# Optimization experiments

Measured on AMD Instinct MI355X. Metric: run time of the kernel, lower is better.

Reference implementation:

```python
import jax, jax.numpy as jnp
from jax import lax
import numpy as np

DN = ('NCHW', 'OIHW', 'NCHW')

def conv(x, w, b, stride, pad):
    y = lax.conv_general_dilated(x, w, (stride, stride), [(pad, pad), (pad, pad)], dimension_numbers=DN)
    return y + b[None, :, None, None]

def conv_t(x, w, b, stride, pad):
    # PyTorch ConvTranspose2d weight layout is (in, out, kh, kw); flip spatially, swap to OIHW,
    # and realize transpose-conv as lhs-dilated conv with padding k-1-p.
    k = w.shape[2]
    wt = jnp.flip(w, (2, 3)).transpose(1, 0, 2, 3)
    q = k - 1 - pad
    y = lax.conv_general_dilated(x, wt, (1, 1), [(q, q), (q, q)], lhs_dilation=(stride, stride), dimension_numbers=DN)
    return y + b[None, :, None, None]

def setup_inputs() -> dict:
    key = jax.random.key(0)
    ks = jax.random.split(key, 16)
    K, C = 512, 64
    def he(k, shape, fan_in):
        return jax.random.normal(k, shape, jnp.float32) * np.float32(np.sqrt(2.0 / fan_in))
    return {
        'x': jax.random.normal(ks[0], (64, 1, 256, 256), jnp.float32),
        'e1_w': he(ks[1], (32, 1, 4, 4), 1 * 16), 'e1_b': jnp.zeros((32,), jnp.float32),
        'e2_w': he(ks[2], (64, 32, 4, 4), 32 * 16), 'e2_b': jnp.zeros((64,), jnp.float32),
        'e3_w': he(ks[3], (64, 64, 3, 3), 64 * 9), 'e3_b': jnp.zeros((64,), jnp.float32),
        'emb': jax.random.uniform(ks[4], (K, C), jnp.float32, -1.0 / K, 1.0 / K),
        'd1_w': he(ks[5], (64, 32, 3, 3), 64 * 9), 'd1_b': jnp.zeros((32,), jnp.float32),
        'd2_w': he(ks[6], (32, 64, 4, 4), 32 * 16), 'd2_b': jnp.zeros((64,), jnp.float32),
        'd3_w': he(ks[7], (64, 1, 4, 4), 64 * 16), 'd3_b': jnp.zeros((1,), jnp.float32),
    }

def reference(x, e1_w, e1_b, e2_w, e2_b, e3_w, e3_b, emb, d1_w, d1_b, d2_w, d2_b, d3_w, d3_b):
    # encoder
    h = jax.nn.relu(conv(x, e1_w, e1_b, 2, 1))
    h = jax.nn.relu(conv(h, e2_w, e2_b, 2, 1))
    ze = jax.nn.relu(conv(h, e3_w, e3_b, 1, 1))  # (N, C, H, W)
    N, C, H, W = ze.shape
    # VQ: nearest codebook entry per spatial location via ||z||^2 - 2 z.e + ||e||^2
    zf = ze.transpose(0, 2, 3, 1).reshape(-1, C)  # (N*H*W, C)
    dist = (zf * zf).sum(-1, keepdims=True) - 2.0 * (zf @ emb.T) + (emb * emb).sum(-1)[None, :]
    idx = jnp.argmin(dist, axis=1)  # (N*H*W,)
    zq = emb[idx].reshape(N, H, W, C).transpose(0, 3, 1, 2)  # (N, C, H, W)
    # straight-through estimator
    dec_in = ze + lax.stop_gradient(zq - ze)
    # decoder
    h = jax.nn.relu(conv_t(dec_in, d1_w, d1_b, 1, 1))
    h = jax.nn.relu(conv_t(h, d2_w, d2_b, 2, 1))
    x_hat = conv_t(h, d3_w, d3_b, 2, 1)
    return (x_hat, ze, zq)
```

## Files before the change

### kernel.cpp

```cpp
#include <hip/hip_runtime.h>

typedef short short8 __attribute__((ext_vector_type(8)));
typedef float f32x4 __attribute__((ext_vector_type(4)));

union U8 { short8 s8; unsigned int u[4]; };

__device__ __forceinline__ unsigned short f2bf(float f) {
    unsigned int u = __float_as_uint(f);
    u = (u + 0x7fffu + ((u >> 16) & 1u)) >> 16;
    return (unsigned short)u;
}
__device__ __forceinline__ float bf2f(unsigned short s) {
    return __uint_as_float(((unsigned int)s) << 16);
}


__global__ __launch_bounds__(256) void k_e1i(
    const float* __restrict__ x, const float* __restrict__ e1w, const float* __restrict__ e1b,
    unsigned short* __restrict__ h1p2, unsigned int* __restrict__ ws_dw,
    const float* __restrict__ e2w, const float* __restrict__ e3w,
    const float* __restrict__ d1w, const float* __restrict__ d2w,
    const float* __restrict__ d3w, const float* __restrict__ emb,
    unsigned short* __restrict__ ape2, unsigned short* __restrict__ ape3,
    unsigned short* __restrict__ apd1, unsigned short* __restrict__ apd2,
    unsigned short* __restrict__ apd3, unsigned short* __restrict__ embbf,
    float* __restrict__ hninit)
{
    int bid = blockIdx.x;
    if (bid < 4096) {
        int idx = bid * 256 + threadIdx.x;
        int ow = idx & 127, oh = (idx >> 7) & 127, n = idx >> 14;
        const float* xn = x + (size_t)n * 65536;
        float patch[16];
#pragma unroll
        for (int kh = 0; kh < 4; kh++) {
            int ih = 2 * oh + kh - 1;
#pragma unroll
            for (int kw = 0; kw < 4; kw++) {
                int iw = 2 * ow + kw - 1;
                bool ok = ((unsigned)ih < 256u) & ((unsigned)iw < 256u);
                patch[kh * 4 + kw] = ok ? xn[ih * 256 + iw] : 0.f;
            }
        }
        unsigned int outw[16];
#pragma unroll
        for (int oc = 0; oc < 32; oc++) {
            float acc = e1b[oc];
#pragma unroll
            for (int t = 0; t < 16; t++) acc += patch[t] * e1w[oc * 16 + t];
            unsigned short bf = f2bf(fmaxf(acc, 0.f));
            if (oc & 1) outw[oc >> 1] |= ((unsigned int)bf) << 16;
            else        outw[oc >> 1] = bf;
        }
        int par = ow & 1;
        int cidx = (ow + par) >> 1;
        size_t base = ((size_t)((idx >> 14) * 130 + oh + 1) * 2 + par) * 2112 + cidx * 32;
        uint4* dst = (uint4*)(h1p2 + base);
#pragma unroll
        for (int i = 0; i < 4; i++) dst[i] = *(uint4*)&outw[i * 4];
        return;
    }
    if (bid < 11376) {
        int t = (bid - 4096) * 256 + threadIdx.x;
        if (t < 270336) {
            int img = t / 4224, q = t % 4224;
            int rowsel = q / 2112, rem = q % 2112;
            ws_dw[img * 274560 + rowsel * 129 * 2112 + rem] = 0u;
        } else if (t < 532480) {
            int g = t - 270336;
            int img = g / 4096, q = g % 4096;
            int row = 1 + (q >> 5), c2 = q & 31;
            int sel = c2 >> 4, ch = c2 & 15;
            int par = sel ? 0 : 1, idx2 = sel ? 64 : 0;
            ws_dw[img * 274560 + row * 2112 + par * 1056 + idx2 * 16 + ch] = 0u;
        } else if (t < 1863680) {
            unsigned int base, Cd, r;
            if (t < 1064960)      { base = 17571840u; Cd = 32; r = t - 532480;  }
            else if (t < 1597440) { base = 34881536u; Cd = 32; r = t - 1064960; }
            else                  { base = 43802624u; Cd = 16; r = t - 1597440; }
            unsigned int per_img = 260u * Cd;
            unsigned int img = r / per_img, q = r % per_img;
            unsigned int p = q / Cd, c = q % Cd;
            unsigned int row, col;
            if (p < 66u)        { row = 0;  col = p; }
            else if (p < 132u)  { row = 65; col = p - 66u; }
            else { unsigned int s = p - 132u; row = 1 + (s >> 1); col = (s & 1) ? 65u : 0u; }
            ws_dw[base + ((img * 66u + row) * 66u + col) * Cd + c] = 0u;
        }
        return;
    }
    int f = (bid - 11376) * 256 + threadIdx.x;
    if (f < 4096) {
        int ks = f >> 8, mt = (f >> 6) & 3, lane = f & 63;
        int quad = lane >> 4, l16 = lane & 15;
        int oc = mt * 16 + l16, kh = ks >> 2, kw = ks & 3;
        short8 sv;
#pragma unroll
        for (int j = 0; j < 8; j++) {
            int ic = quad * 8 + j;
            sv[j] = (short)f2bf(e2w[((oc * 32 + ic) * 4 + kh) * 4 + kw]);
        }
        ((short8*)ape2)[f] = sv;
    } else if (f < 8704) {
        int g = f - 4096;
        int ks = g >> 8, mt = (g >> 6) & 3, lane = g & 63;
        int quad = lane >> 4, l16 = lane & 15;
        int oc = mt * 16 + l16, tap = ks >> 1, kh = tap / 3, kw = tap % 3;
        int icb = (ks & 1) * 32 + quad * 8;
        short8 sv;
#pragma unroll
        for (int j = 0; j < 8; j++)
            sv[j] = (short)f2bf(e3w[((oc * 64 + icb + j) * 3 + kh) * 3 + kw]);
        ((short8*)ape3)[g] = sv;
    } else if (f < 11008) {
        int g = f - 8704;
        int ks = g >> 7, mt = (g >> 6) & 1, lane = g & 63;
        int quad = lane >> 4, l16 = lane & 15;
        int oc = mt * 16 + l16, tap = ks >> 1, kh = tap / 3, kw = tap % 3;
        int icb = (ks & 1) * 32 + quad * 8;
        short8 sv;
#pragma unroll
        for (int j = 0; j < 8; j++)
            sv[j] = (short)f2bf(d1w[(((icb + j) * 32 + oc) * 3 + (2 - kh)) * 3 + (2 - kw)]);
        ((short8*)apd1)[g] = sv;
    } else if (f < 15104) {
        int g = f - 11008;
        int par = g >> 10, ks = (g >> 8) & 3, mt = (g >> 6) & 3, lane = g & 63;
        int quad = lane >> 4, l16 = lane & 15;
        int ph = par >> 1, pw = par & 1, a = ks >> 1, bb = ks & 1;
        int kh = 3 - ph - 2 * a, kw = 3 - pw - 2 * bb;
        int oc = mt * 16 + l16;
        short8 sv;
#pragma unroll
        for (int j = 0; j < 8; j++) {
            int ic = quad * 8 + j;
            sv[j] = (short)f2bf(d2w[((ic * 64 + oc) * 4 + kh) * 4 + kw]);
        }
        ((short8*)apd2)[g] = sv;
    } else if (f < 15232) {
        int g = f - 15104;
        int ks = g >> 6, lane = g & 63;
        int quad = lane >> 4, tap = lane & 15;
        short8 sv;
#pragma unroll
        for (int j = 0; j < 8; j++) {
            int ic = ks * 32 + quad * 8 + j;
            sv[j] = (short)f2bf(d3w[ic * 16 + tap]);
        }
        ((short8*)apd3)[g] = sv;
    } else if (f < 19328) {
        int g = f - 15232;
        int code = g >> 3, chb = (g & 7) * 8;
        short8 sv;
#pragma unroll
        for (int j = 0; j < 8; j++) sv[j] = (short)f2bf(emb[code * 64 + chb + j]);
        ((short8*)embbf)[g] = sv;
    } else if (f < 19840) {
        int code = f - 19328;
        float s = 0.f;
        for (int c = 0; c < 64; c++) { float v = emb[code * 64 + c]; s += v * v; }
        hninit[code] = 2.0f - 0.5f * s;
    }
}

template<int CIN, int COUT, int KSTEPS, int NCH, int WPIN, int MODE>
__global__ __launch_bounds__(256, 4) void k_conv(const unsigned short* __restrict__ inp,
                                                 const unsigned short* __restrict__ aprep,
                                                 const float* __restrict__ bias,
                                                 unsigned short* __restrict__ out0) {
    constexpr int MT = COUT / 16;
    constexpr int KCH = KSTEPS / NCH;
    __shared__ short8 sA[KCH * MT * 64];
    int tid = threadIdx.x;
    int wave = tid >> 6, lane = tid & 63, quad = lane >> 4, l16 = lane & 15;
    int bid = blockIdx.x;
    int n = bid >> 4, rg = bid & 15;
    int oh = rg * 4 + wave;

    int base0;
    if (MODE == 0) base0 = (n * 130 + 2 * oh) * 4224 + quad * 8;
    else           base0 = n * (WPIN * WPIN * CIN) + ((oh + 1) * WPIN + 1) * CIN + quad * 8;

    f32x4 acc[4][MT];
#pragma unroll
    for (int t = 0; t < 4; t++)
#pragma unroll
        for (int mt = 0; mt < MT; mt++)
            acc[t][mt] = *(const f32x4*)(bias + mt * 16 + quad * 4);

#pragma unroll
    for (int ch = 0; ch < NCH; ch++) {
        for (int i = tid; i < KCH * MT * 64; i += 256)
            sA[i] = ((const short8*)aprep)[ch * (KCH * MT * 64) + i];
        __syncthreads();
#pragma unroll
        for (int k = 0; k < KCH; k++) {
            int ks = ch * KCH + k;
            int off, pxs;
            if (MODE == 0) {
                int kh = ks >> 2, kw = ks & 3;
                int par = (kw & 1) ^ 1;
                off = kh * 4224 + par * 2112 + (kw >> 1) * 32;
                pxs = 32;
            } else {
                int tap = ks >> 1, kh = tap / 3, kw = tap % 3;
                off = ((kh - 1) * WPIN + (kw - 1)) * CIN + (ks & 1) * 32;
                pxs = CIN;
            }
            short8 bfr[4];
#pragma unroll
            for (int t = 0; t < 4; t++)
                bfr[t] = *(const short8*)(inp + base0 + (t * 16 + l16) * pxs + off);
#pragma unroll
            for (int mt = 0; mt < MT; mt++) {
                short8 a = sA[(k * MT + mt) * 64 + lane];
#pragma unroll
                for (int t = 0; t < 4; t++)
                    acc[t][mt] = __builtin_amdgcn_mfma_f32_16x16x32_bf16(a, bfr[t], acc[t][mt], 0, 0, 0);
            }
        }
        if (ch + 1 < NCH) __syncthreads();
    }

#pragma unroll
    for (int t = 0; t < 4; t++) {
        int ow = t * 16 + l16;
#pragma unroll
        for (int mt = 0; mt < MT; mt++) {
            float v0 = fmaxf(acc[t][mt][0], 0.f), v1 = fmaxf(acc[t][mt][1], 0.f);
            float v2 = fmaxf(acc[t][mt][2], 0.f), v3 = fmaxf(acc[t][mt][3], 0.f);
            unsigned int lo = (unsigned int)f2bf(v0) | ((unsigned int)f2bf(v1) << 16);
            unsigned int hi = (unsigned int)f2bf(v2) | ((unsigned int)f2bf(v3) << 16);
            uint2 uu; uu.x = lo; uu.y = hi;
            int oc = mt * 16 + quad * 4;
            if (MODE == 0) {
                size_t addr = (size_t)n * 278784 + ((oh + 1) * 66 + ow + 1) * 64 + oc;
                *(uint2*)(out0 + addr) = uu;
            } else {
                size_t addr = (size_t)n * 139392 + ((oh + 1) * 66 + ow + 1) * 32 + oc;
                *(uint2*)(out0 + addr) = uu;
            }
        }
    }
}

__global__ __launch_bounds__(256, 5) void k_e3vq(const unsigned short* __restrict__ h2p,
                                                 const unsigned short* __restrict__ ape3,
                                                 const float* __restrict__ bias,
                                                 const unsigned short* __restrict__ embbf,
                                                 const float* __restrict__ hninit,
                                                 float* __restrict__ ze_out,
                                                 float* __restrict__ zq_out,
                                                 unsigned short* __restrict__ zqp) {
    int tid = threadIdx.x;
    int wave = tid >> 6, lane = tid & 63, quad = lane >> 4, l16 = lane & 15;
    int bid = blockIdx.x;
    int n = bid >> 5, rg = (bid >> 1) & 15, half = bid & 1;
    int oh = rg * 4 + wave;
    int c0 = half * 32;
    int base0 = n * 278784 + ((oh + 1) * 66 + 1 + c0) * 64 + quad * 8;
    const short8* A = (const short8*)ape3;

    f32x4 acc[2][4];
#pragma unroll
    for (int t = 0; t < 2; t++)
#pragma unroll
        for (int mt = 0; mt < 4; mt++)
            acc[t][mt] = *(const f32x4*)(bias + mt * 16 + quad * 4);

#pragma unroll
    for (int ks = 0; ks < 18; ks++) {
        int tap = ks >> 1, kh = tap / 3, kw = tap % 3;
        int off = ((kh - 1) * 66 + (kw - 1)) * 64 + (ks & 1) * 32;
        short8 bfr[2];
#pragma unroll
        for (int t = 0; t < 2; t++)
            bfr[t] = *(const short8*)(h2p + base0 + (t * 16 + l16) * 64 + off);
#pragma unroll
        for (int mt = 0; mt < 4; mt++) {
            short8 a = A[(ks * 4 + mt) * 64 + lane];
#pragma unroll
            for (int t = 0; t < 2; t++)
                acc[t][mt] = __builtin_amdgcn_mfma_f32_16x16x32_bf16(a, bfr[t], acc[t][mt], 0, 0, 0);
        }
    }

#pragma unroll
    for (int t = 0; t < 2; t++)
#pragma unroll
        for (int mt = 0; mt < 4; mt++)
#pragma unroll
            for (int r = 0; r < 4; r++)
                acc[t][mt][r] = fmaxf(acc[t][mt][r], 0.f);

#pragma unroll
    for (int t = 0; t < 2; t++) {
        int px = oh * 64 + c0 + t * 16 + l16;
#pragma unroll
        for (int mt = 0; mt < 4; mt++) {
            int oc = mt * 16 + quad * 4;
#pragma unroll
            for (int r = 0; r < 4; r++)
                __builtin_nontemporal_store(acc[t][mt][r], &ze_out[((size_t)n * 64 + oc + r) * 4096 + px]);
        }
    }

    short8 b0[2], b1[2];
    int s0 = (((2 * quad) & 3) << 4) | l16;
    int s1 = (((2 * quad + 1) & 3) << 4) | l16;
#pragma unroll
    for (int t = 0; t < 2; t++) {
        f32x4 xv = (quad < 2) ? acc[t][0] : acc[t][1];
        f32x4 yv = (quad < 2) ? acc[t][2] : acc[t][3];
        unsigned int xa = (unsigned int)f2bf(xv[0]) | ((unsigned int)f2bf(xv[1]) << 16);
        unsigned int xb = (unsigned int)f2bf(xv[2]) | ((unsigned int)f2bf(xv[3]) << 16);
        unsigned int ya = (unsigned int)f2bf(yv[0]) | ((unsigned int)f2bf(yv[1]) << 16);
        unsigned int yb = (unsigned int)f2bf(yv[2]) | ((unsigned int)f2bf(yv[3]) << 16);
        U8 ub0, ub1;
        ub0.u[0] = (unsigned int)__shfl((int)xa, s0); ub0.u[1] = (unsigned int)__shfl((int)xb, s0);
        ub0.u[2] = (unsigned int)__shfl((int)xa, s1); ub0.u[3] = (unsigned int)__shfl((int)xb, s1);
        ub1.u[0] = (unsigned int)__shfl((int)ya, s0); ub1.u[1] = (unsigned int)__shfl((int)yb, s0);
        ub1.u[2] = (unsigned int)__shfl((int)ya, s1); ub1.u[3] = (unsigned int)__shfl((int)yb, s1);
        b0[t] = ub0.s8; b1[t] = ub1.s8;
    }

    unsigned int bk[2] = {0u, 0u};
#pragma unroll 4
    for (int j0 = 0; j0 < 512; j0 += 16) {
        short8 a0 = *(const short8*)(embbf + (j0 + l16) * 64 + quad * 8);
        short8 a1 = *(const short8*)(embbf + (j0 + l16) * 64 + 32 + quad * 8);
        f32x4 ci = *(const f32x4*)(hninit + j0 + quad * 4);
        int iv = 511 - j0 - quad * 4;
#pragma unroll
        for (int t = 0; t < 2; t++) {
            f32x4 s = __builtin_amdgcn_mfma_f32_16x16x32_bf16(a0, b0[t], ci, 0, 0, 0);
            s = __builtin_amdgcn_mfma_f32_16x16x32_bf16(a1, b1[t], s, 0, 0, 0);
#pragma unroll
            for (int r = 0; r < 4; r++) {
                unsigned int key = (__float_as_uint(s[r]) & 0xFFFFFE00u) | (unsigned int)(iv - r);
                bk[t] = bk[t] > key ? bk[t] : key;
            }
        }
    }
#pragma unroll
    for (int t = 0; t < 2; t++) {
        unsigned int o1 = (unsigned int)__shfl_xor((int)bk[t], 16);
        bk[t] = bk[t] > o1 ? bk[t] : o1;
        unsigned int o2 = (unsigned int)__shfl_xor((int)bk[t], 32);
        bk[t] = bk[t] > o2 ? bk[t] : o2;
    }
#pragma unroll
    for (int t = 0; t < 2; t++) {
        int code = 511 - (int)(bk[t] & 511u);
        int col = c0 + t * 16 + l16;
        int hw = oh * 64 + col;
        uint4 u0 = *(const uint4*)(embbf + code * 64 + quad * 16);
        uint4 u1 = *(const uint4*)(embbf + code * 64 + quad * 16 + 8);
        size_t qaddr = (size_t)n * 278784 + ((oh + 1) * 66 + (col + 1)) * 64 + quad * 16;
        *(uint4*)(zqp + qaddr) = u0;
        *(uint4*)(zqp + qaddr + 8) = u1;
        size_t zb = ((size_t)n * 64 + quad * 16) * 4096 + hw;
        unsigned int uw[8] = {u0.x, u0.y, u0.z, u0.w, u1.x, u1.y, u1.z, u1.w};
#pragma unroll
        for (int i = 0; i < 8; i++) {
            __builtin_nontemporal_store(__uint_as_float(uw[i] << 16), &zq_out[zb + (2 * i + 0) * 4096]);
            __builtin_nontemporal_store(__uint_as_float(uw[i] & 0xFFFF0000u), &zq_out[zb + (2 * i + 1) * 4096]);
        }
    }
}

__global__ __launch_bounds__(256, 4) void k_d2f(const unsigned short* __restrict__ d1op,
                                                const unsigned short* __restrict__ apd2,
                                                const float* __restrict__ bias,
                                                const unsigned short* __restrict__ apd3,
                                                unsigned short* __restrict__ sc16) {
    __shared__ short8 sA[1024];
    int tid = threadIdx.x;
    int wave = tid >> 6, lane = tid & 63, quad = lane >> 4, l16 = lane & 15;
    int bid = blockIdx.x;
    int n = bid >> 6, par = (bid >> 4) & 3, rg = bid & 15;
    int oh = rg * 4 + wave;
    int ph = par >> 1, pw = par & 1;

    short8 pa0 = ((const short8*)apd3)[lane];
    short8 pa1 = ((const short8*)apd3)[64 + lane];

    for (int i = tid; i < 1024; i += 256) sA[i] = ((const short8*)apd2)[par * 1024 + i];
    __syncthreads();

    int base0 = n * 139392 + ((oh + ph) * 66 + pw) * 32 + quad * 8;
    f32x4 acc[4][4];
#pragma unroll
    for (int t = 0; t < 4; t++)
#pragma unroll
        for (int mt = 0; mt < 4; mt++)
            acc[t][mt] = *(const f32x4*)(bias + mt * 16 + quad * 4);

#pragma unroll
    for (int k = 0; k < 4; k++) {
        int a_ = k >> 1, bb = k & 1;
        int off = (a_ * 66 + bb) * 32;
        short8 bfr[4];
#pragma unroll
        for (int t = 0; t < 4; t++)
            bfr[t] = *(const short8*)(d1op + base0 + (t * 16 + l16) * 32 + off);
#pragma unroll
        for (int mt = 0; mt < 4; mt++) {
            short8 a = sA[(k * 4 + mt) * 64 + lane];
#pragma unroll
            for (int t = 0; t < 4; t++)
                acc[t][mt] = __builtin_amdgcn_mfma_f32_16x16x32_bf16(a, bfr[t], acc[t][mt], 0, 0, 0);
        }
    }

    int s0 = (((2 * quad) & 3) << 4) | l16;
    int s1 = (((2 * quad + 1) & 3) << 4) | l16;
    int oh_out = 2 * oh + ph;
#pragma unroll
    for (int t = 0; t < 4; t++) {
#pragma unroll
        for (int mt = 0; mt < 4; mt++)
#pragma unroll
            for (int r = 0; r < 4; r++)
                acc[t][mt][r] = fmaxf(acc[t][mt][r], 0.f);
        f32x4 xv = (quad < 2) ? acc[t][0] : acc[t][1];
        f32x4 yv = (quad < 2) ? acc[t][2] : acc[t][3];
        unsigned int xa = (unsigned int)f2bf(xv[0]) | ((unsigned int)f2bf(xv[1]) << 16);
        unsigned int xb = (unsigned int)f2bf(xv[2]) | ((unsigned int)f2bf(xv[3]) << 16);
        unsigned int ya = (unsigned int)f2bf(yv[0]) | ((unsigned int)f2bf(yv[1]) << 16);
        unsigned int yb = (unsigned int)f2bf(yv[2]) | ((unsigned int)f2bf(yv[3]) << 16);
        U8 ub0, ub1;
        ub0.u[0] = (unsigned int)__shfl((int)xa, s0); ub0.u[1] = (unsigned int)__shfl((int)xb, s0);
        ub0.u[2] = (unsigned int)__shfl((int)xa, s1); ub0.u[3] = (unsigned int)__shfl((int)xb, s1);
        ub1.u[0] = (unsigned int)__shfl((int)ya, s0); ub1.u[1] = (unsigned int)__shfl((int)yb, s0);
        ub1.u[2] = (unsigned int)__shfl((int)ya, s1); ub1.u[3] = (unsigned int)__shfl((int)yb, s1);
        f32x4 sc = {0.f, 0.f, 0.f, 0.f};
        sc = __builtin_amdgcn_mfma_f32_16x16x32_bf16(pa0, ub0.s8, sc, 0, 0, 0);
        sc = __builtin_amdgcn_mfma_f32_16x16x32_bf16(pa1, ub1.s8, sc, 0, 0, 0);
        int ow_out = 2 * (t * 16 + l16) + pw;
        int pbaseo = n * 16384 + oh_out * 128 + ow_out;
#pragma unroll
        for (int r = 0; r < 4; r++) {
            int tap = quad * 4 + r;
            sc16[(size_t)tap * 1048576 + pbaseo] = f2bf(sc[r]);
        }
    }
}

__global__ __launch_bounds__(256) void k_d3e(const unsigned short* __restrict__ sc16,
                                             const float* __restrict__ d3b,
                                             float* __restrict__ xhat) {
    int idx = blockIdx.x * 256 + threadIdx.x;
    int ow = idx & 255, oh = (idx >> 8) & 255, n = idx >> 16;
    float acc = d3b[0];
    int kh0 = (oh + 1) & 1, kw0 = (ow + 1) & 1;
#pragma unroll
    for (int dh = 0; dh < 2; dh++) {
        int kh = kh0 + 2 * dh;
        int ih = (oh + 1 - kh) >> 1;
        bool vh = ((unsigned)ih < 128u);
#pragma unroll
        for (int dw = 0; dw < 2; dw++) {
            int kw = kw0 + 2 * dw;
            int iw = (ow + 1 - kw) >> 1;
            if (vh && ((unsigned)iw < 128u))
                acc += bf2f(sc16[(size_t)(kh * 4 + kw) * 1048576 + n * 16384 + ih * 128 + iw]);
        }
    }
    __builtin_nontemporal_store(acc, &xhat[(size_t)n * 65536 + oh * 256 + ow]);
}

extern "C" void kernel_launch(void* const* d_in, const int* in_sizes, int n_in,
                              void* d_out, int out_size, void* d_ws, size_t ws_size,
                              hipStream_t stream) {
    const float* x    = (const float*)d_in[0];
    const float* e1w  = (const float*)d_in[1];
    const float* e1b  = (const float*)d_in[2];
    const float* e2w  = (const float*)d_in[3];
    const float* e2b  = (const float*)d_in[4];
    const float* e3w  = (const float*)d_in[5];
    const float* e3b  = (const float*)d_in[6];
    const float* emb  = (const float*)d_in[7];
    const float* d1w  = (const float*)d_in[8];
    const float* d1b  = (const float*)d_in[9];
    const float* d2w  = (const float*)d_in[10];
    const float* d2b  = (const float*)d_in[11];
    const float* d3w  = (const float*)d_in[12];
    const float* d3b  = (const float*)d_in[13];

    float* xhat = (float*)d_out;
    float* ze   = xhat + 4194304;
    float* zq   = ze + 16777216;

    char* ws = (char*)d_ws;
    unsigned short* h1p2   = (unsigned short*)(ws + 0);
    unsigned short* h2p    = (unsigned short*)(ws + 70287360);
    unsigned short* zqp    = (unsigned short*)(ws + 139526144);
    unsigned short* d1op   = (unsigned short*)(ws + 175210496);
    unsigned short* sc16   = (unsigned short*)(ws + 193052672);
    unsigned short* ape2   = (unsigned short*)(ws + 226607104);
    unsigned short* ape3   = (unsigned short*)(ws + 226672640);
    unsigned short* apd1   = (unsigned short*)(ws + 226746368);
    unsigned short* apd2   = (unsigned short*)(ws + 226783232);
    unsigned short* apd3   = (unsigned short*)(ws + 226848768);
    unsigned short* embbf  = (unsigned short*)(ws + 226850816);
    float*          hninit = (float*)(ws + 226916352);

    k_e1i<<<11454, 256, 0, stream>>>(x, e1w, e1b, h1p2, (unsigned int*)d_ws,
                                     e2w, e3w, d1w, d2w, d3w, emb,
                                     ape2, ape3, apd1, apd2, apd3, embbf, hninit);
    k_conv<32, 64, 16, 2, 0, 0><<<1024, 256, 0, stream>>>(h1p2, ape2, e2b, h2p);
    k_e3vq<<<2048, 256, 0, stream>>>(h2p, ape3, e3b, embbf, hninit, ze, zq, zqp);
    k_conv<64, 32, 18, 2, 66, 2><<<1024, 256, 0, stream>>>(zqp, apd1, d1b, d1op);
    k_d2f<<<4096, 256, 0, stream>>>(d1op, apd2, d2b, apd3, sc16);
    k_d3e<<<16384, 256, 0, stream>>>(sc16, d3b, xhat);
}
```

Measured before the change: 457.9 us.

## Stage e3 weights and VQ codebook through shared memory in k_e3vq

After: 407.0 us. 1.13x faster.

```diff
diff --git a/kernel.cpp b/kernel.cpp
--- a/kernel.cpp
+++ b/kernel.cpp
@@ -252,6 +252,10 @@
                                                  float* __restrict__ ze_out,
                                                  float* __restrict__ zq_out,
                                                  unsigned short* __restrict__ zqp) {
+    __shared__ __align__(16) char smem[24576];
+    short8* sA = (short8*)smem;
+    char*   sC = smem;
+
     int tid = threadIdx.x;
     int wave = tid >> 6, lane = tid & 63, quad = lane >> 4, l16 = lane & 15;
     int bid = blockIdx.x;
@@ -259,7 +263,6 @@
     int oh = rg * 4 + wave;
     int c0 = half * 32;
     int base0 = n * 278784 + ((oh + 1) * 66 + 1 + c0) * 64 + quad * 8;
-    const short8* A = (const short8*)ape3;
 
     f32x4 acc[2][4];
 #pragma unroll
@@ -269,19 +272,27 @@
             acc[t][mt] = *(const f32x4*)(bias + mt * 16 + quad * 4);
 
 #pragma unroll
-    for (int ks = 0; ks < 18; ks++) {
-        int tap = ks >> 1, kh = tap / 3, kw = tap % 3;
-        int off = ((kh - 1) * 66 + (kw - 1)) * 64 + (ks & 1) * 32;
-        short8 bfr[2];
-#pragma unroll
-        for (int t = 0; t < 2; t++)
-            bfr[t] = *(const short8*)(h2p + base0 + (t * 16 + l16) * 64 + off);
-#pragma unroll
-        for (int mt = 0; mt < 4; mt++) {
-            short8 a = A[(ks * 4 + mt) * 64 + lane];
+    for (int ch = 0; ch < 3; ch++) {
+        if (ch) __syncthreads();
+        for (int i = tid; i < 6 * 4 * 64; i += 256)
+            sA[i] = ((const short8*)ape3)[ch * (6 * 4 * 64) + i];
+        __syncthreads();
+#pragma unroll
+        for (int k = 0; k < 6; k++) {
+            int ks = ch * 6 + k;
+            int tap = ks >> 1, kh = tap / 3, kw = tap % 3;
+            int off = ((kh - 1) * 66 + (kw - 1)) * 64 + (ks & 1) * 32;
+            short8 bfr[2];
 #pragma unroll
             for (int t = 0; t < 2; t++)
-                acc[t][mt] = __builtin_amdgcn_mfma_f32_16x16x32_bf16(a, bfr[t], acc[t][mt], 0, 0, 0);
+                bfr[t] = *(const short8*)(h2p + base0 + (t * 16 + l16) * 64 + off);
+#pragma unroll
+            for (int mt = 0; mt < 4; mt++) {
+                short8 a = sA[(k * 4 + mt) * 64 + lane];
+#pragma unroll
+                for (int t = 0; t < 2; t++)
+                    acc[t][mt] = __builtin_amdgcn_mfma_f32_16x16x32_bf16(a, bfr[t], acc[t][mt], 0, 0, 0);
+            }
         }
     }
 
@@ -325,20 +336,38 @@
     }
 
     unsigned int bk[2] = {0u, 0u};
-#pragma unroll 4
-    for (int j0 = 0; j0 < 512; j0 += 16) {
-        short8 a0 = *(const short8*)(embbf + (j0 + l16) * 64 + quad * 8);
-        short8 a1 = *(const short8*)(embbf + (j0 + l16) * 64 + 32 + quad * 8);
-        f32x4 ci = *(const f32x4*)(hninit + j0 + quad * 4);
-        int iv = 511 - j0 - quad * 4;
-#pragma unroll
-        for (int t = 0; t < 2; t++) {
-            f32x4 s = __builtin_amdgcn_mfma_f32_16x16x32_bf16(a0, b0[t], ci, 0, 0, 0);
-            s = __builtin_amdgcn_mfma_f32_16x16x32_bf16(a1, b1[t], s, 0, 0, 0);
-#pragma unroll
-            for (int r = 0; r < 4; r++) {
-                unsigned int key = (__float_as_uint(s[r]) & 0xFFFFFE00u) | (unsigned int)(iv - r);
-                bk[t] = bk[t] > key ? bk[t] : key;
+#pragma unroll 1
+    for (int cb = 0; cb < 4; cb++) {
+        __syncthreads();
+        {
+            int r = tid >> 1, h = tid & 1;
+            const uint4* src = (const uint4*)embbf;
+#pragma unroll
+            for (int i = 0; i < 4; i++) {
+                uint4 v = src[cb * 1024 + tid * 4 + i];
+                int slot = 4 * h + i;
+                *(uint4*)(sC + r * 128 + ((slot ^ (r & 7)) << 4)) = v;
+            }
+        }
+        __syncthreads();
+#pragma unroll 2
+        for (int jj = 0; jj < 8; jj++) {
+            int j0 = cb * 128 + jj * 16;
+            int rr = jj * 16 + l16;
+            int sw = (rr & 7) << 4;
+            short8 a0 = *(const short8*)(sC + rr * 128 + (((quad << 4)) ^ sw));
+            short8 a1 = *(const short8*)(sC + rr * 128 + ((((quad + 4) << 4)) ^ sw));
+            f32x4 ci = *(const f32x4*)(hninit + j0 + quad * 4);
+            int iv = 511 - j0 - quad * 4;
+#pragma unroll
+            for (int t = 0; t < 2; t++) {
+                f32x4 s = __builtin_amdgcn_mfma_f32_16x16x32_bf16(a0, b0[t], ci, 0, 0, 0);
+                s = __builtin_amdgcn_mfma_f32_16x16x32_bf16(a1, b1[t], s, 0, 0, 0);
+#pragma unroll
+                for (int r = 0; r < 4; r++) {
+                    unsigned int key = (__float_as_uint(s[r]) & 0xFFFFFE00u) | (unsigned int)(iv - r);
+                    bk[t] = bk[t] > key ? bk[t] : key;
+                }
             }
         }
     }
```
